# Optimization experiments

Measured on AMD Instinct MI355X. Metric: run time of the kernel, lower is better.

Reference implementation:

```python
import jax, jax.numpy as jnp
import numpy as np

D_MODEL = 1024
NUM_HEADS = 16
D_K = D_MODEL // NUM_HEADS
ROPE_THETA = 10000.0


def setup_inputs() -> dict:
    key = jax.random.key(0)
    kx, kq, kk, kv, ko = jax.random.split(key, 5)
    B, S = 4, 2048
    std = (2.0 / (D_MODEL + D_MODEL)) ** 0.5
    def w(k):
        return jax.random.truncated_normal(k, -3.0, 3.0, (D_MODEL, D_MODEL), jnp.float32) * std
    return {
        "x": jax.random.normal(kx, (B, S, D_MODEL), jnp.float32),
        "Wq": w(kq), "Wk": w(kk), "Wv": w(kv), "Wo": w(ko),
    }


def _apply_rope(t):
    # t: [B, H, S, d_k]
    S, dk = t.shape[-2], t.shape[-1]
    inv_freq = 1.0 / (ROPE_THETA ** (jnp.arange(0, dk, 2) / dk))  # [dk/2]
    angles = jnp.outer(jnp.arange(S), inv_freq)                    # [S, dk/2]
    cos = jnp.repeat(jnp.cos(angles), 2, axis=-1).astype(t.dtype)  # [S, dk]
    sin = jnp.repeat(jnp.sin(angles), 2, axis=-1).astype(t.dtype)
    t_even = t[..., 0::2]
    t_odd = t[..., 1::2]
    t_rot = jnp.stack([-t_odd, t_even], axis=-1).reshape(t.shape)
    return t * cos + t_rot * sin


def reference(x, Wq, Wk, Wv, Wo):
    B, S, D = x.shape
    H, dk = NUM_HEADS, D_K
    q = jnp.einsum("bsi,io->bso", x, Wq).reshape(B, S, H, dk).swapaxes(1, 2)
    k = jnp.einsum("bsi,io->bso", x, Wk).reshape(B, S, H, dk).swapaxes(1, 2)
    v = jnp.einsum("bsi,io->bso", x, Wv).reshape(B, S, H, dk).swapaxes(1, 2)
    q = _apply_rope(q)
    k = _apply_rope(k)
    scores = jnp.einsum("bhqd,bhkd->bhqk", q, k) / (dk ** 0.5)  # [B,H,S,S]
    causal = jnp.tril(jnp.ones((S, S), dtype=bool))
    scores = jnp.where(causal, scores, -jnp.inf)
    attn = jax.nn.softmax(scores, axis=-1)
    out = jnp.einsum("bhqk,bhkd->bhqd", attn, v)  # [B,H,S,dk]
    out = out.swapaxes(1, 2).reshape(B, S, D)
    return jnp.einsum("bsi,io->bso", out, Wo)
```

## Files before the change

### kernel.cpp

```cpp
#include <hip/hip_runtime.h>
#include <hip/hip_bf16.h>

#define SEQ   2048
#define NB    4
#define NH    16
#define DK    64
#define DM    1024
#define MROWS (NB * SEQ)

typedef __bf16 bf16_t;
typedef __bf16 bf16x8 __attribute__((ext_vector_type(8)));
typedef __bf16 bf16x4 __attribute__((ext_vector_type(4)));
typedef float  f32x4  __attribute__((ext_vector_type(4)));

#define MFMA16(a, b, c) __builtin_amdgcn_mfma_f32_16x16x32_bf16((a), (b), (c), 0, 0, 0)

__device__ __forceinline__ void gl2lds16(const bf16_t* g, bf16_t* l) {
    __builtin_amdgcn_global_load_lds(
        (const __attribute__((address_space(1))) unsigned int*)g,
        (__attribute__((address_space(3))) unsigned int*)l, 16, 0, 0);
}

#define BAR()   __builtin_amdgcn_s_barrier()
#define SCB()   __builtin_amdgcn_sched_barrier(0)
#define LGK0()  asm volatile("s_waitcnt lgkmcnt(0)")
#define LGK8()  asm volatile("s_waitcnt lgkmcnt(8)")
#define VMC(N)  asm volatile("s_waitcnt vmcnt(" #N ")")

__global__ __launch_bounds__(256) void cvt_kernel(
    const float* __restrict__ in, bf16_t* __restrict__ out, int n)
{
    int i = (blockIdx.x * 256 + threadIdx.x) * 4;
    if (i + 3 < n) {
        const float4 v = *(const float4*)(in + i);
        bf16x4 o;
        o[0] = (bf16_t)v.x; o[1] = (bf16_t)v.y;
        o[2] = (bf16_t)v.z; o[3] = (bf16_t)v.w;
        *(bf16x4*)(out + i) = o;
    }
}

__global__ __launch_bounds__(256) void wtr_kernel(
    const float* __restrict__ W, bf16_t* __restrict__ Wt)
{
    __shared__ float T[32][33];
    const int tk0 = (blockIdx.x >> 5) << 5;
    const int tn0 = (blockIdx.x & 31) << 5;
    const int r = threadIdx.x >> 5, c = threadIdx.x & 31;
#pragma unroll
    for (int i = 0; i < 4; ++i)
        T[r + i * 8][c] = W[(size_t)(tk0 + r + i * 8) * DM + tn0 + c];
    __syncthreads();
#pragma unroll
    for (int i = 0; i < 4; ++i)
        Wt[(size_t)(tn0 + r + i * 8) * DM + tk0 + c] = (bf16_t)T[c][r + i * 8];
}

__global__ void rope_table_kernel(float2* __restrict__ tab) {
    int idx = blockIdx.x * 256 + threadIdx.x;
    if (idx >= SEQ * 32) return;
    int s = idx >> 5, i = idx & 31;
    float freq = powf(10000.0f, -(float)i / 32.0f);
    float a = (float)s * freq;
    tab[idx] = make_float2(cosf(a), sinf(a));
}

template<bool TR>
__device__ __forceinline__ void kloop(
    const bf16_t* __restrict__ Xp, const bf16_t* __restrict__ Wp,
    bf16_t* L, int tid, f32x4 (&acc)[8][4])
{
    const int lane = tid & 63;
    const int wave = tid >> 6;
    const int wm   = wave >> 2;
    const int wn   = wave & 3;
    const int lrow = lane & 15;
    const int lcol = (lane >> 4) << 3;

    bf16_t* const AR = L;
    bf16_t* const BR = L + 32768;

    const bf16_t* pA0 = Xp + (size_t)(wave * 16 + lrow) * DM + lcol;
    const bf16_t* pA1 = pA0 + (size_t)128 * DM;
    const bf16_t* pB0 = Wp + (size_t)(wave * 16 + lrow) * DM + lcol;
    const bf16_t* pB1 = pB0 + (size_t)128 * DM;

    bf16_t* const adst = AR + wave * 1024;
    bf16_t* const bdst = BR + wave * 1024;

    const bf16_t* const Ard = AR + wm * 8192;
    const bf16_t* const Brd = BR + wn * 4096;

    bf16x8 a[2][2], bc[4][2];

#define RD_A(BUF, Q)                                                          \
    a[0][0] = *(const bf16x8*)(Ard + (BUF) + (2*(Q)+0)*1024 + lane*8);        \
    a[0][1] = *(const bf16x8*)(Ard + (BUF) + (2*(Q)+0)*1024 + 512 + lane*8);  \
    a[1][0] = *(const bf16x8*)(Ard + (BUF) + (2*(Q)+1)*1024 + lane*8);        \
    a[1][1] = *(const bf16x8*)(Ard + (BUF) + (2*(Q)+1)*1024 + 512 + lane*8);

#define RD_B(BUF, NF)                                                         \
    bc[NF][0] = *(const bf16x8*)(Brd + (BUF) + (NF)*1024 + lane*8);           \
    bc[NF][1] = *(const bf16x8*)(Brd + (BUF) + (NF)*1024 + 512 + lane*8);

#define ST_A(BUF, H, C)                                                       \
    gl2lds16(((H) ? pA1 : pA0) + (C),      adst + (BUF) + (H)*8192);          \
    gl2lds16(((H) ? pA1 : pA0) + (C) + 32, adst + (BUF) + (H)*8192 + 512);

#define ST_B(BUF, H, C)                                                       \
    gl2lds16(((H) ? pB1 : pB0) + (C),      bdst + (BUF) + (H)*8192);          \
    gl2lds16(((H) ? pB1 : pB0) + (C) + 32, bdst + (BUF) + (H)*8192 + 512);

#define QMMA(Q)                                                               \
    __builtin_amdgcn_s_setprio(1);                                            \
    _Pragma("unroll")                                                         \
    for (int nf = 0; nf < 4; ++nf) {                                          \
        if (TR) {                                                             \
            acc[2*(Q)][nf]   = MFMA16(bc[nf][0], a[0][0], acc[2*(Q)][nf]);    \
            acc[2*(Q)][nf]   = MFMA16(bc[nf][1], a[0][1], acc[2*(Q)][nf]);    \
            acc[2*(Q)+1][nf] = MFMA16(bc[nf][0], a[1][0], acc[2*(Q)+1][nf]);  \
            acc[2*(Q)+1][nf] = MFMA16(bc[nf][1], a[1][1], acc[2*(Q)+1][nf]);  \
        } else {                                                              \
            acc[2*(Q)][nf]   = MFMA16(a[0][0], bc[nf][0], acc[2*(Q)][nf]);    \
            acc[2*(Q)][nf]   = MFMA16(a[0][1], bc[nf][1], acc[2*(Q)][nf]);    \
            acc[2*(Q)+1][nf] = MFMA16(a[1][0], bc[nf][0], acc[2*(Q)+1][nf]);  \
            acc[2*(Q)+1][nf] = MFMA16(a[1][1], bc[nf][1], acc[2*(Q)+1][nf]);  \
        }                                                                     \
    }                                                                         \
    __builtin_amdgcn_s_setprio(0);

    ST_B(0, 0, 0)      ST_B(0, 1, 0)
    ST_A(0, 0, 0)      ST_A(0, 1, 0)
    ST_B(16384, 0, 64) ST_B(16384, 1, 64)
    VMC(4);
    BAR();

    for (int it = 0; it < 8; ++it) {
        const bool lst = (it == 7);

        RD_A(0, 0) RD_B(0, 0) RD_B(0, 1) RD_B(0, 2) RD_B(0, 3)
        ST_A(16384, 0, 64) ST_A(16384, 1, 64)
        LGK8();
        BAR(); LGK0(); SCB();
        QMMA(0)
        BAR();

        RD_A(0, 1)
        if (!lst) { ST_B(0, 0, 128) }
        BAR(); LGK0(); SCB();
        QMMA(1)
        BAR();

        RD_A(0, 2)
        if (!lst) { ST_B(0, 1, 128) }
        BAR(); LGK0(); SCB();
        QMMA(2)
        BAR();

        RD_A(0, 3)
        BAR(); LGK0(); SCB();
        QMMA(3)
        if (lst) { VMC(0); } else { VMC(4); }
        BAR();

        RD_A(16384, 0) RD_B(16384, 0) RD_B(16384, 1) RD_B(16384, 2) RD_B(16384, 3)
        if (!lst) { ST_A(0, 0, 128) }
        LGK8();
        BAR(); LGK0(); SCB();
        QMMA(0)
        BAR();

        RD_A(16384, 1)
        if (!lst) { ST_A(0, 1, 128) }
        BAR(); LGK0(); SCB();
        QMMA(1)
        BAR();

        RD_A(16384, 2)
        if (!lst) { ST_B(16384, 0, 192) }
        BAR(); LGK0(); SCB();
        QMMA(2)
        BAR();

        RD_A(16384, 3)
        if (!lst) { ST_B(16384, 1, 192) }
        BAR(); LGK0(); SCB();
        QMMA(3)
        if (!lst) { VMC(4); }
        BAR();

        pA0 += 128; pA1 += 128; pB0 += 128; pB1 += 128;
    }

#undef QMMA
#undef ST_B
#undef ST_A
#undef RD_B
#undef RD_A
}

__global__ __launch_bounds__(512, 2) void gemm_qkv_kernel(
    const bf16_t* __restrict__ X, const bf16_t* __restrict__ Wt,
    bf16_t* __restrict__ Qt, bf16_t* __restrict__ Kt, bf16_t* __restrict__ Vtr,
    const float2* __restrict__ rope)
{
    __shared__ __align__(16) bf16_t L[65536];

    const int tid = threadIdx.x;
    const int xcd = blockIdx.x & 7;
    const int idx = blockIdx.x >> 3;
    const int mt  = xcd * 4 + (idx & 3);
    const int nt  = idx >> 2;
    const int m0 = mt << 8, n0 = nt << 8;
    const bool tr = (n0 >= 2 * DM);

    f32x4 acc[8][4] = {};
    if (tr) kloop<true >(X + (size_t)m0 * DM, Wt + (size_t)n0 * DM, L, tid, acc);
    else    kloop<false>(X + (size_t)m0 * DM, Wt + (size_t)n0 * DM, L, tid, acc);

    const int lane = tid & 63;
    const int wave = tid >> 6;
    const int wm   = wave >> 2, wn = wave & 3;
    const int l    = lane & 15;
    const int quad = lane >> 4;

#pragma unroll
    for (int mf = 0; mf < 8; ++mf)
#pragma unroll
        for (int nf = 0; nf < 4; ++nf)
#pragma unroll
            for (int r = 0; r < 4; ++r) {
                float v = acc[mf][nf][r];
                if (tr) {
                    const int n = n0 + wn * 64 + nf * 16 + quad * 4 + r;
                    const int m = m0 + wm * 128 + mf * 16 + l;
                    const int bi = m >> 11, s = m & (SEQ - 1);
                    const int col = n & (DM - 1);
                    const int h = col >> 6, d = col & (DK - 1);
                    Vtr[(((size_t)(bi * NH + h)) * DK + d) * SEQ + s] = (bf16_t)v;
                } else {
                    const int m  = m0 + wm * 128 + mf * 16 + quad * 4 + r;
                    const int nn = n0 + wn * 64 + nf * 16 + l;
                    const int bi = m >> 11, s = m & (SEQ - 1);
                    const int col = nn & (DM - 1);
                    const int h = col >> 6, d = col & (DK - 1);
                    float pv = __shfl_xor(v, 1);
                    float2 cs = rope[s * 32 + (d >> 1)];
                    float res = (d & 1) ? (v * cs.x + pv * cs.y)
                                        : (v * cs.x - pv * cs.y);
                    bf16_t* dst = (nn < DM) ? Qt : Kt;
                    if (nn < DM) res *= 0.125f;
                    dst[(((size_t)(bi * NH + h)) * SEQ + s) * DK + d] = (bf16_t)res;
                }
            }
}

__global__ __launch_bounds__(512, 2) void gemm_out_kernel(
    const bf16_t* __restrict__ X, const bf16_t* __restrict__ Wt,
    float* __restrict__ out)
{
    __shared__ __align__(16) bf16_t L[65536];

    const int tid = threadIdx.x;
    const int xcd = blockIdx.x & 7;
    const int idx = blockIdx.x >> 3;
    const int mt  = xcd * 4 + (idx & 3);
    const int nt  = idx >> 2;
    const int m0 = mt << 8, n0 = nt << 8;

    f32x4 acc[8][4] = {};
    kloop<false>(X + (size_t)m0 * DM, Wt + (size_t)n0 * DM, L, tid, acc);

    const int lane = tid & 63;
    const int wave = tid >> 6;
    const int wm   = wave >> 2, wn = wave & 3;
    const int l    = lane & 15;
    const int quad = lane >> 4;

#pragma unroll
    for (int mf = 0; mf < 8; ++mf)
#pragma unroll
        for (int nf = 0; nf < 4; ++nf)
#pragma unroll
            for (int r = 0; r < 4; ++r) {
                const int m  = m0 + wm * 128 + mf * 16 + quad * 4 + r;
                const int nn = n0 + wn * 64 + nf * 16 + l;
                out[(size_t)m * DM + nn] = acc[mf][nf][r];
            }
}

#define KLD 72

__global__ __launch_bounds__(256) void attn_kernel(
    const bf16_t* __restrict__ Q, const bf16_t* __restrict__ K,
    const bf16_t* __restrict__ Vt, bf16_t* __restrict__ O)
{
    __shared__ __align__(16) bf16_t Kl[64 * KLD];
    __shared__ __align__(16) bf16_t Vl[64 * KLD];
    __shared__ __align__(16) bf16_t Pl[4][32 * KLD];

    const int bh   = blockIdx.x;
    const int qx   = blockIdx.y;
    const int tid  = threadIdx.x;
    const int wave = tid >> 6;
    const int lane = tid & 63;
    const int l    = lane & 15;
    const int quad = lane >> 4;
    const int srow = tid >> 3;
    const int sch  = (tid & 7) << 3;

    bf16_t* Pw = Pl[wave];
    const bf16_t* Qb = Q  + (size_t)bh * SEQ * DK;
    const bf16_t* Kb = K  + (size_t)bh * SEQ * DK;
    const bf16_t* Vb = Vt + (size_t)bh * DK * SEQ;
    const int b = bh >> 4, h = bh & 15;

    for (int ph = 0; ph < 2; ++ph) {
        const int qblk = ph ? (15 - qx) : qx;
        const int q0w  = qblk * 128 + wave * 32;
        const int nch  = 2 * (qblk + 1);

        bf16x8 qb[2][2];
#pragma unroll
        for (int u = 0; u < 2; ++u) {
            qb[u][0] = *(const bf16x8*)(Qb + (size_t)(q0w + u * 16 + l) * DK + quad * 8);
            qb[u][1] = *(const bf16x8*)(Qb + (size_t)(q0w + u * 16 + l) * DK + 32 + quad * 8);
        }

        float m_run[2] = {-3e38f, -3e38f};
        float l_run[2] = {0.f, 0.f};
        f32x4 o[4][2] = {};

        bf16x8 pk0 = *(const bf16x8*)(Kb + (size_t)srow * DK + sch);
        bf16x8 pk1 = *(const bf16x8*)(Kb + (size_t)(32 + srow) * DK + sch);
        bf16x8 pv0 = *(const bf16x8*)(Vb + (size_t)srow * SEQ + sch);
        bf16x8 pv1 = *(const bf16x8*)(Vb + (size_t)(32 + srow) * SEQ + sch);

        for (int i = 0; i < nch; ++i) {
            const int c = i * 64;
            __syncthreads();
            *(bf16x8*)(Kl + srow * KLD + sch)        = pk0;
            *(bf16x8*)(Kl + (32 + srow) * KLD + sch) = pk1;
            *(bf16x8*)(Vl + srow * KLD + sch)        = pv0;
            *(bf16x8*)(Vl + (32 + srow) * KLD + sch) = pv1;
            __syncthreads();
            if (i + 1 < nch) {
                const int cn = c + 64;
                pk0 = *(const bf16x8*)(Kb + (size_t)(cn + srow) * DK + sch);
                pk1 = *(const bf16x8*)(Kb + (size_t)(cn + 32 + srow) * DK + sch);
                pv0 = *(const bf16x8*)(Vb + (size_t)srow * SEQ + cn + sch);
                pv1 = *(const bf16x8*)(Vb + (size_t)(32 + srow) * SEQ + cn + sch);
            }
            if (c > q0w + 31) continue;

            f32x4 st[4][2] = {};
#pragma unroll
            for (int t = 0; t < 4; ++t) {
                const bf16x8 k0 = *(const bf16x8*)(Kl + (t * 16 + l) * KLD + quad * 8);
                const bf16x8 k1 = *(const bf16x8*)(Kl + (t * 16 + l) * KLD + 32 + quad * 8);
                st[t][0] = MFMA16(k0, qb[0][0], st[t][0]);
                st[t][0] = MFMA16(k1, qb[0][1], st[t][0]);
                st[t][1] = MFMA16(k0, qb[1][0], st[t][1]);
                st[t][1] = MFMA16(k1, qb[1][1], st[t][1]);
            }
            if (c + 63 > q0w) {
#pragma unroll
                for (int u = 0; u < 2; ++u) {
                    const int thr = q0w + u * 16 + l - c - quad * 4;
#pragma unroll
                    for (int t = 0; t < 4; ++t)
#pragma unroll
                        for (int r = 0; r < 4; ++r)
                            if (t * 16 + r > thr) st[t][u][r] = -3e38f;
                }
            }
#pragma unroll
            for (int u = 0; u < 2; ++u) {
                float cmax = -3e38f;
#pragma unroll
                for (int t = 0; t < 4; ++t)
#pragma unroll
                    for (int r = 0; r < 4; ++r)
                        cmax = fmaxf(cmax, st[t][u][r]);
                cmax = fmaxf(cmax, __shfl_xor(cmax, 16));
                cmax = fmaxf(cmax, __shfl_xor(cmax, 32));
                const float mnew  = fmaxf(m_run[u], cmax);
                const float alpha = __expf(m_run[u] - mnew);
                m_run[u] = mnew;
                float csum = 0.f;
#pragma unroll
                for (int t = 0; t < 4; ++t)
#pragma unroll
                    for (int r = 0; r < 4; ++r) {
                        st[t][u][r] = __expf(st[t][u][r] - mnew);
                        csum += st[t][u][r];
                    }
                csum += __shfl_xor(csum, 16);
                csum += __shfl_xor(csum, 32);
                l_run[u] = l_run[u] * alpha + csum;
#pragma unroll
                for (int n = 0; n < 4; ++n)
#pragma unroll
                    for (int r = 0; r < 4; ++r)
                        o[n][u][r] *= alpha;
#pragma unroll
                for (int t = 0; t < 4; ++t) {
                    bf16x4 pk;
                    pk[0] = (bf16_t)st[t][u][0]; pk[1] = (bf16_t)st[t][u][1];
                    pk[2] = (bf16_t)st[t][u][2]; pk[3] = (bf16_t)st[t][u][3];
                    *(bf16x4*)(Pw + (u * 16 + l) * KLD + t * 16 + quad * 4) = pk;
                }
            }
            const bf16x8 pb00 = *(const bf16x8*)(Pw + l * KLD + quad * 8);
            const bf16x8 pb01 = *(const bf16x8*)(Pw + l * KLD + 32 + quad * 8);
            const bf16x8 pb10 = *(const bf16x8*)(Pw + (16 + l) * KLD + quad * 8);
            const bf16x8 pb11 = *(const bf16x8*)(Pw + (16 + l) * KLD + 32 + quad * 8);
#pragma unroll
            for (int n = 0; n < 4; ++n) {
                const bf16x8 v0 = *(const bf16x8*)(Vl + (n * 16 + l) * KLD + quad * 8);
                const bf16x8 v1 = *(const bf16x8*)(Vl + (n * 16 + l) * KLD + 32 + quad * 8);
                o[n][0] = MFMA16(v0, pb00, o[n][0]);
                o[n][0] = MFMA16(v1, pb01, o[n][0]);
                o[n][1] = MFMA16(v0, pb10, o[n][1]);
                o[n][1] = MFMA16(v1, pb11, o[n][1]);
            }
        }

#pragma unroll
        for (int u = 0; u < 2; ++u) {
            const float inv = 1.0f / l_run[u];
#pragma unroll
            for (int n = 0; n < 4; ++n) {
                bf16x4 ov;
                ov[0] = (bf16_t)(o[n][u][0] * inv); ov[1] = (bf16_t)(o[n][u][1] * inv);
                ov[2] = (bf16_t)(o[n][u][2] * inv); ov[3] = (bf16_t)(o[n][u][3] * inv);
                *(bf16x4*)(Pw + (u * 16 + l) * KLD + n * 16 + quad * 4) = ov;
            }
        }
        const int row  = lane >> 1;
        const int half = (lane & 1) * 32;
        const bf16x8 w0 = *(const bf16x8*)(Pw + row * KLD + half);
        const bf16x8 w1 = *(const bf16x8*)(Pw + row * KLD + half + 8);
        const bf16x8 w2 = *(const bf16x8*)(Pw + row * KLD + half + 16);
        const bf16x8 w3 = *(const bf16x8*)(Pw + row * KLD + half + 24);
        bf16_t* op = O + ((size_t)(b * SEQ + qblk * 128 + wave * 32 + row)) * DM
                       + h * DK + half;
        *(bf16x8*)(op)      = w0;
        *(bf16x8*)(op + 8)  = w1;
        *(bf16x8*)(op + 16) = w2;
        *(bf16x8*)(op + 24) = w3;
    }
}

extern "C" void kernel_launch(void* const* d_in, const int* in_sizes, int n_in,
                              void* d_out, int out_size, void* d_ws, size_t ws_size,
                              hipStream_t stream)
{
    const float* x  = (const float*)d_in[0];
    const float* Wq = (const float*)d_in[1];
    const float* Wk = (const float*)d_in[2];
    const float* Wv = (const float*)d_in[3];
    const float* Wo = (const float*)d_in[4];

    char* ws = (char*)d_ws;
    float2* rope = (float2*)ws;
    const size_t TEN = (size_t)MROWS * DM;
    const size_t WEL = (size_t)DM * DM;
    bf16_t* xb    = (bf16_t*)(ws + (1 << 19));
    bf16_t* Wqkvt = xb + TEN;
    bf16_t* Wot   = Wqkvt + 3 * WEL;
    bf16_t* Qt    = Wot + WEL;
    bf16_t* Kt    = Qt + TEN;
    bf16_t* Vt    = Kt + TEN;
    bf16_t* Ot    = Vt + TEN;

    rope_table_kernel<<<(SEQ * 32 + 255) / 256, 256, 0, stream>>>(rope);

    cvt_kernel<<<(int)(TEN / 4 / 256), 256, 0, stream>>>(x, xb, (int)TEN);
    wtr_kernel<<<1024, 256, 0, stream>>>(Wq, Wqkvt);
    wtr_kernel<<<1024, 256, 0, stream>>>(Wk, Wqkvt + WEL);
    wtr_kernel<<<1024, 256, 0, stream>>>(Wv, Wqkvt + 2 * WEL);
    wtr_kernel<<<1024, 256, 0, stream>>>(Wo, Wot);

    gemm_qkv_kernel<<<32 * 12, 512, 0, stream>>>(xb, Wqkvt, Qt, Kt, Vt, rope);

    attn_kernel<<<dim3(NB * NH, 8), 256, 0, stream>>>(Qt, Kt, Vt, Ot);

    gemm_out_kernel<<<32 * 4, 512, 0, stream>>>(Ot, Wot, (float*)d_out);
}
```

Baseline: 310.3 us.

## Merge prep kernels, halve output GEMM tile, double-buffer attention K/V

Replaces the six setup launches (rope table, x conversion, four weight transposes) with a single prep kernel that dispatches on block index. The output projection GEMM moves from 256x256 to 128x256 tiles with its own inlined pipelined k-loop, doubling the block count from 128 to 256 so more CUs are busy. The attention kernel double-buffers K/V in shared memory so it needs one barrier per chunk instead of two. The costs are more LDS in attention, less reuse per block in the output GEMM, and a more complex hand-written barrier/waitcnt schedule.

```diff
diff --git a/kernel.cpp b/kernel.cpp
--- a/kernel.cpp
+++ b/kernel.cpp
@@ -7,6 +7,7 @@
 #define DK    64
 #define DM    1024
 #define MROWS (NB * SEQ)
+#define WEL   (DM * DM)
 
 typedef __bf16 bf16_t;
 typedef __bf16 bf16x8 __attribute__((ext_vector_type(8)));
@@ -27,42 +28,47 @@
 #define LGK8()  asm volatile("s_waitcnt lgkmcnt(8)")
 #define VMC(N)  asm volatile("s_waitcnt vmcnt(" #N ")")
 
-__global__ __launch_bounds__(256) void cvt_kernel(
-    const float* __restrict__ in, bf16_t* __restrict__ out, int n)
+__global__ __launch_bounds__(256) void prep_kernel(
+    const float* __restrict__ x,
+    const float* __restrict__ Wq, const float* __restrict__ Wk,
+    const float* __restrict__ Wv, const float* __restrict__ Wo,
+    bf16_t* __restrict__ xb, bf16_t* __restrict__ Wqkvt,
+    bf16_t* __restrict__ Wot, float2* __restrict__ rope)
 {
-    int i = (blockIdx.x * 256 + threadIdx.x) * 4;
-    if (i + 3 < n) {
-        const float4 v = *(const float4*)(in + i);
+    __shared__ float T[32][33];
+    const int bid = blockIdx.x;
+    const int tid = threadIdx.x;
+
+    if (bid < 8192) {
+        const int i = (bid * 256 + tid) * 4;
+        const float4 v = *(const float4*)(x + i);
         bf16x4 o;
         o[0] = (bf16_t)v.x; o[1] = (bf16_t)v.y;
         o[2] = (bf16_t)v.z; o[3] = (bf16_t)v.w;
-        *(bf16x4*)(out + i) = o;
+        *(bf16x4*)(xb + i) = o;
+    } else if (bid < 12288) {
+        const int wb = bid - 8192;
+        const int w  = wb >> 10;
+        const int b10 = wb & 1023;
+        const float* W = (w == 0) ? Wq : (w == 1) ? Wk : (w == 2) ? Wv : Wo;
+        bf16_t* Wt = (w == 3) ? Wot : Wqkvt + (size_t)w * WEL;
+        const int tk0 = (b10 >> 5) << 5;
+        const int tn0 = (b10 & 31) << 5;
+        const int r = tid >> 5, c = tid & 31;
+#pragma unroll
+        for (int i = 0; i < 4; ++i)
+            T[r + i * 8][c] = W[(size_t)(tk0 + r + i * 8) * DM + tn0 + c];
+        __syncthreads();
+#pragma unroll
+        for (int i = 0; i < 4; ++i)
+            Wt[(size_t)(tn0 + r + i * 8) * DM + tk0 + c] = (bf16_t)T[c][r + i * 8];
+    } else {
+        const int idx = (bid - 12288) * 256 + tid;
+        const int s = idx >> 5, i = idx & 31;
+        const float freq = powf(10000.0f, -(float)i / 32.0f);
+        const float a = (float)s * freq;
+        rope[idx] = make_float2(cosf(a), sinf(a));
     }
-}
-
-__global__ __launch_bounds__(256) void wtr_kernel(
-    const float* __restrict__ W, bf16_t* __restrict__ Wt)
-{
-    __shared__ float T[32][33];
-    const int tk0 = (blockIdx.x >> 5) << 5;
-    const int tn0 = (blockIdx.x & 31) << 5;
-    const int r = threadIdx.x >> 5, c = threadIdx.x & 31;
-#pragma unroll
-    for (int i = 0; i < 4; ++i)
-        T[r + i * 8][c] = W[(size_t)(tk0 + r + i * 8) * DM + tn0 + c];
-    __syncthreads();
-#pragma unroll
-    for (int i = 0; i < 4; ++i)
-        Wt[(size_t)(tn0 + r + i * 8) * DM + tk0 + c] = (bf16_t)T[c][r + i * 8];
-}
-
-__global__ void rope_table_kernel(float2* __restrict__ tab) {
-    int idx = blockIdx.x * 256 + threadIdx.x;
-    if (idx >= SEQ * 32) return;
-    int s = idx >> 5, i = idx & 31;
-    float freq = powf(10000.0f, -(float)i / 32.0f);
-    float a = (float)s * freq;
-    tab[idx] = make_float2(cosf(a), sinf(a));
 }
 
 template<bool TR>
@@ -259,44 +265,136 @@
     const bf16_t* __restrict__ X, const bf16_t* __restrict__ Wt,
     float* __restrict__ out)
 {
-    __shared__ __align__(16) bf16_t L[65536];
+    __shared__ __align__(16) bf16_t L[49152];
 
     const int tid = threadIdx.x;
     const int xcd = blockIdx.x & 7;
     const int idx = blockIdx.x >> 3;
-    const int mt  = xcd * 4 + (idx & 3);
-    const int nt  = idx >> 2;
-    const int m0 = mt << 8, n0 = nt << 8;
-
-    f32x4 acc[8][4] = {};
-    kloop<false>(X + (size_t)m0 * DM, Wt + (size_t)n0 * DM, L, tid, acc);
+    const int mt  = xcd * 8 + (idx & 7);
+    const int nt  = idx >> 3;
+    const int m0 = mt << 7, n0 = nt << 8;
 
     const int lane = tid & 63;
     const int wave = tid >> 6;
-    const int wm   = wave >> 2, wn = wave & 3;
+    const int wm   = wave >> 2;
+    const int wn   = wave & 3;
+    const int lrow = lane & 15;
+    const int lcol = (lane >> 4) << 3;
+
+    bf16_t* const AR = L;
+    bf16_t* const BR = L + 16384;
+
+    const bf16_t* Xp = X + (size_t)m0 * DM;
+    const bf16_t* Wp = Wt + (size_t)n0 * DM;
+    const bf16_t* pA  = Xp + (size_t)(wave * 16 + lrow) * DM + lcol;
+    const bf16_t* pB0 = Wp + (size_t)(wave * 16 + lrow) * DM + lcol;
+    const bf16_t* pB1 = pB0 + (size_t)128 * DM;
+
+    bf16_t* const adst = AR + wave * 1024;
+    bf16_t* const bdst = BR + wave * 1024;
+
+    const bf16_t* const Ard = AR + wm * 4096;
+    const bf16_t* const Brd = BR + wn * 4096;
+
+    f32x4 acc[4][4] = {};
+    bf16x8 a[2][2], bc[4][2];
+
+#define RD_AH(BUF, Q)                                                         \
+    a[0][0] = *(const bf16x8*)(Ard + (BUF) + (2*(Q)+0)*1024 + lane*8);        \
+    a[0][1] = *(const bf16x8*)(Ard + (BUF) + (2*(Q)+0)*1024 + 512 + lane*8);  \
+    a[1][0] = *(const bf16x8*)(Ard + (BUF) + (2*(Q)+1)*1024 + lane*8);        \
+    a[1][1] = *(const bf16x8*)(Ard + (BUF) + (2*(Q)+1)*1024 + 512 + lane*8);
+
+#define RD_BH(BUF, NF)                                                        \
+    bc[NF][0] = *(const bf16x8*)(Brd + (BUF) + (NF)*1024 + lane*8);           \
+    bc[NF][1] = *(const bf16x8*)(Brd + (BUF) + (NF)*1024 + 512 + lane*8);
+
+#define ST_AH(BUF, C)                                                         \
+    gl2lds16(pA + (C),      adst + (BUF));                                    \
+    gl2lds16(pA + (C) + 32, adst + (BUF) + 512);
+
+#define ST_BH(BUF, H, C)                                                      \
+    gl2lds16(((H) ? pB1 : pB0) + (C),      bdst + (BUF) + (H)*8192);          \
+    gl2lds16(((H) ? pB1 : pB0) + (C) + 32, bdst + (BUF) + (H)*8192 + 512);
+
+#define QMMAH(Q)                                                              \
+    __builtin_amdgcn_s_setprio(1);                                            \
+    _Pragma("unroll")                                                         \
+    for (int nf = 0; nf < 4; ++nf) {                                          \
+        acc[2*(Q)][nf]   = MFMA16(a[0][0], bc[nf][0], acc[2*(Q)][nf]);        \
+        acc[2*(Q)][nf]   = MFMA16(a[0][1], bc[nf][1], acc[2*(Q)][nf]);        \
+        acc[2*(Q)+1][nf] = MFMA16(a[1][0], bc[nf][0], acc[2*(Q)+1][nf]);      \
+        acc[2*(Q)+1][nf] = MFMA16(a[1][1], bc[nf][1], acc[2*(Q)+1][nf]);      \
+    }                                                                         \
+    __builtin_amdgcn_s_setprio(0);
+
+    ST_AH(0, 0)
+    ST_BH(0, 0, 0) ST_BH(0, 1, 0)
+    ST_BH(16384, 0, 64) ST_BH(16384, 1, 64)
+    VMC(4);
+    BAR();
+
+    for (int it = 0; it < 8; ++it) {
+        const bool lst = (it == 7);
+
+        RD_AH(0, 0) RD_BH(0, 0) RD_BH(0, 1) RD_BH(0, 2) RD_BH(0, 3)
+        ST_AH(8192, 64)
+        LGK8();
+        BAR(); LGK0(); SCB();
+        QMMAH(0)
+        BAR();
+        RD_AH(0, 1)
+        if (!lst) { ST_BH(0, 0, 128) ST_BH(0, 1, 128) }
+        BAR(); LGK0(); SCB();
+        QMMAH(1)
+        if (lst) { VMC(0); } else { VMC(4); }
+        BAR();
+
+        RD_AH(8192, 0) RD_BH(16384, 0) RD_BH(16384, 1) RD_BH(16384, 2) RD_BH(16384, 3)
+        if (!lst) { ST_AH(0, 128) }
+        LGK8();
+        BAR(); LGK0(); SCB();
+        QMMAH(0)
+        BAR();
+        RD_AH(8192, 1)
+        if (!lst) { ST_BH(16384, 0, 192) ST_BH(16384, 1, 192) }
+        BAR(); LGK0(); SCB();
+        QMMAH(1)
+        if (!lst) { VMC(4); }
+        BAR();
+
+        pA += 128; pB0 += 128; pB1 += 128;
+    }
+
+#undef QMMAH
+#undef ST_BH
+#undef ST_AH
+#undef RD_BH
+#undef RD_AH
+
     const int l    = lane & 15;
     const int quad = lane >> 4;
-
-#pragma unroll
-    for (int mf = 0; mf < 8; ++mf)
+#pragma unroll
+    for (int mf = 0; mf < 4; ++mf)
 #pragma unroll
         for (int nf = 0; nf < 4; ++nf)
 #pragma unroll
             for (int r = 0; r < 4; ++r) {
-                const int m  = m0 + wm * 128 + mf * 16 + quad * 4 + r;
+                const int m  = m0 + wm * 64 + mf * 16 + quad * 4 + r;
                 const int nn = n0 + wn * 64 + nf * 16 + l;
                 out[(size_t)m * DM + nn] = acc[mf][nf][r];
             }
 }
 
-#define KLD 72
+#define KLD  72
+#define KVSZ (64 * KLD)
 
 __global__ __launch_bounds__(256) void attn_kernel(
     const bf16_t* __restrict__ Q, const bf16_t* __restrict__ K,
     const bf16_t* __restrict__ Vt, bf16_t* __restrict__ O)
 {
-    __shared__ __align__(16) bf16_t Kl[64 * KLD];
-    __shared__ __align__(16) bf16_t Vl[64 * KLD];
+    __shared__ __align__(16) bf16_t Kl[2 * KVSZ];
+    __shared__ __align__(16) bf16_t Vl[2 * KVSZ];
     __shared__ __align__(16) bf16_t Pl[4][32 * KLD];
 
     const int bh   = blockIdx.x;
@@ -335,95 +433,111 @@
         bf16x8 pk1 = *(const bf16x8*)(Kb + (size_t)(32 + srow) * DK + sch);
         bf16x8 pv0 = *(const bf16x8*)(Vb + (size_t)srow * SEQ + sch);
         bf16x8 pv1 = *(const bf16x8*)(Vb + (size_t)(32 + srow) * SEQ + sch);
+        __syncthreads();
+        *(bf16x8*)(Kl + srow * KLD + sch)        = pk0;
+        *(bf16x8*)(Kl + (32 + srow) * KLD + sch) = pk1;
+        *(bf16x8*)(Vl + srow * KLD + sch)        = pv0;
+        *(bf16x8*)(Vl + (32 + srow) * KLD + sch) = pv1;
+        __syncthreads();
 
         for (int i = 0; i < nch; ++i) {
-            const int c = i * 64;
-            __syncthreads();
-            *(bf16x8*)(Kl + srow * KLD + sch)        = pk0;
-            *(bf16x8*)(Kl + (32 + srow) * KLD + sch) = pk1;
-            *(bf16x8*)(Vl + srow * KLD + sch)        = pv0;
-            *(bf16x8*)(Vl + (32 + srow) * KLD + sch) = pv1;
-            __syncthreads();
-            if (i + 1 < nch) {
+            const int c  = i * 64;
+            const int bf = (i & 1) * KVSZ;
+            const int bn = ((i & 1) ^ 1) * KVSZ;
+            const bool pf = (i + 1 < nch);
+
+            if (pf) {
                 const int cn = c + 64;
                 pk0 = *(const bf16x8*)(Kb + (size_t)(cn + srow) * DK + sch);
                 pk1 = *(const bf16x8*)(Kb + (size_t)(cn + 32 + srow) * DK + sch);
                 pv0 = *(const bf16x8*)(Vb + (size_t)srow * SEQ + cn + sch);
                 pv1 = *(const bf16x8*)(Vb + (size_t)(32 + srow) * SEQ + cn + sch);
             }
-            if (c > q0w + 31) continue;
-
-            f32x4 st[4][2] = {};
-#pragma unroll
-            for (int t = 0; t < 4; ++t) {
-                const bf16x8 k0 = *(const bf16x8*)(Kl + (t * 16 + l) * KLD + quad * 8);
-                const bf16x8 k1 = *(const bf16x8*)(Kl + (t * 16 + l) * KLD + 32 + quad * 8);
-                st[t][0] = MFMA16(k0, qb[0][0], st[t][0]);
-                st[t][0] = MFMA16(k1, qb[0][1], st[t][0]);
-                st[t][1] = MFMA16(k0, qb[1][0], st[t][1]);
-                st[t][1] = MFMA16(k1, qb[1][1], st[t][1]);
-            }
-            if (c + 63 > q0w) {
+
+            if (c <= q0w + 31) {
+                const bf16_t* Klb = Kl + bf;
+                const bf16_t* Vlb = Vl + bf;
+
+                f32x4 st[4][2] = {};
+#pragma unroll
+                for (int t = 0; t < 4; ++t) {
+                    const bf16x8 k0 = *(const bf16x8*)(Klb + (t * 16 + l) * KLD + quad * 8);
+                    const bf16x8 k1 = *(const bf16x8*)(Klb + (t * 16 + l) * KLD + 32 + quad * 8);
+                    st[t][0] = MFMA16(k0, qb[0][0], st[t][0]);
+                    st[t][0] = MFMA16(k1, qb[0][1], st[t][0]);
+                    st[t][1] = MFMA16(k0, qb[1][0], st[t][1]);
+                    st[t][1] = MFMA16(k1, qb[1][1], st[t][1]);
+                }
+                if (c + 63 > q0w) {
+#pragma unroll
+                    for (int u = 0; u < 2; ++u) {
+                        const int thr = q0w + u * 16 + l - c - quad * 4;
+#pragma unroll
+                        for (int t = 0; t < 4; ++t)
+#pragma unroll
+                            for (int r = 0; r < 4; ++r)
+                                if (t * 16 + r > thr) st[t][u][r] = -3e38f;
+                    }
+                }
 #pragma unroll
                 for (int u = 0; u < 2; ++u) {
-                    const int thr = q0w + u * 16 + l - c - quad * 4;
+                    float cmax = -3e38f;
 #pragma unroll
                     for (int t = 0; t < 4; ++t)
 #pragma unroll
                         for (int r = 0; r < 4; ++r)
-                            if (t * 16 + r > thr) st[t][u][r] = -3e38f;
+                            cmax = fmaxf(cmax, st[t][u][r]);
+                    cmax = fmaxf(cmax, __shfl_xor(cmax, 16));
+                    cmax = fmaxf(cmax, __shfl_xor(cmax, 32));
+                    const float mnew  = fmaxf(m_run[u], cmax);
+                    const float alpha = __expf(m_run[u] - mnew);
+                    m_run[u] = mnew;
+                    float csum = 0.f;
+#pragma unroll
+                    for (int t = 0; t < 4; ++t)
+#pragma unroll
+                        for (int r = 0; r < 4; ++r) {
+                            st[t][u][r] = __expf(st[t][u][r] - mnew);
+                            csum += st[t][u][r];
+                        }
+                    csum += __shfl_xor(csum, 16);
+                    csum += __shfl_xor(csum, 32);
+                    l_run[u] = l_run[u] * alpha + csum;
+#pragma unroll
+                    for (int n = 0; n < 4; ++n)
+#pragma unroll
+                        for (int r = 0; r < 4; ++r)
+                            o[n][u][r] *= alpha;
+#pragma unroll
+                    for (int t = 0; t < 4; ++t) {
+                        bf16x4 pk;
+                        pk[0] = (bf16_t)st[t][u][0]; pk[1] = (bf16_t)st[t][u][1];
+                        pk[2] = (bf16_t)st[t][u][2]; pk[3] = (bf16_t)st[t][u][3];
+                        *(bf16x4*)(Pw + (u * 16 + l) * KLD + t * 16 + quad * 4) = pk;
+                    }
+                }
+                const bf16x8 pb00 = *(const bf16x8*)(Pw + l * KLD + quad * 8);
+                const bf16x8 pb01 = *(const bf16x8*)(Pw + l * KLD + 32 + quad * 8);
+                const bf16x8 pb10 = *(const bf16x8*)(Pw + (16 + l) * KLD + quad * 8);
+                const bf16x8 pb11 = *(const bf16x8*)(Pw + (16 + l) * KLD + 32 + quad * 8);
+#pragma unroll
+                for (int n = 0; n < 4; ++n) {
+                    const bf16x8 v0 = *(const bf16x8*)(Vlb + (n * 16 + l) * KLD + quad * 8);
+                    const bf16x8 v1 = *(const bf16x8*)(Vlb + (n * 16 + l) * KLD + 32 + quad * 8);
+                    o[n][0] = MFMA16(v0, pb00, o[n][0]);
+                    o[n][0] = MFMA16(v1, pb01, o[n][0]);
+                    o[n][1] = MFMA16(v0, pb10, o[n][1]);
+                    o[n][1] = MFMA16(v1, pb11, o[n][1]);
                 }
             }
-#pragma unroll
-            for (int u = 0; u < 2; ++u) {
-                float cmax = -3e38f;
-#pragma unroll
-                for (int t = 0; t < 4; ++t)
-#pragma unroll
-                    for (int r = 0; r < 4; ++r)
-                        cmax = fmaxf(cmax, st[t][u][r]);
-                cmax = fmaxf(cmax, __shfl_xor(cmax, 16));
-                cmax = fmaxf(cmax, __shfl_xor(cmax, 32));
-                const float mnew  = fmaxf(m_run[u], cmax);
-                const float alpha = __expf(m_run[u] - mnew);
-                m_run[u] = mnew;
-                float csum = 0.f;
-#pragma unroll
-                for (int t = 0; t < 4; ++t)
-#pragma unroll
-                    for (int r = 0; r < 4; ++r) {
-                        st[t][u][r] = __expf(st[t][u][r] - mnew);
-                        csum += st[t][u][r];
-                    }
-                csum += __shfl_xor(csum, 16);
-                csum += __shfl_xor(csum, 32);
-                l_run[u] = l_run[u] * alpha + csum;
-#pragma unroll
-                for (int n = 0; n < 4; ++n)
-#pragma unroll
-                    for (int r = 0; r < 4; ++r)
-                        o[n][u][r] *= alpha;
-#pragma unroll
-                for (int t = 0; t < 4; ++t) {
-                    bf16x4 pk;
-                    pk[0] = (bf16_t)st[t][u][0]; pk[1] = (bf16_t)st[t][u][1];
-                    pk[2] = (bf16_t)st[t][u][2]; pk[3] = (bf16_t)st[t][u][3];
-                    *(bf16x4*)(Pw + (u * 16 + l) * KLD + t * 16 + quad * 4) = pk;
-                }
+
+            if (pf) {
+                *(bf16x8*)(Kl + bn + srow * KLD + sch)        = pk0;
+                *(bf16x8*)(Kl + bn + (32 + srow) * KLD + sch) = pk1;
+                *(bf16x8*)(Vl + bn + srow * KLD + sch)        = pv0;
+                *(bf16x8*)(Vl + bn + (32 + srow) * KLD + sch) = pv1;
             }
-            const bf16x8 pb00 = *(const bf16x8*)(Pw + l * KLD + quad * 8);
-            const bf16x8 pb01 = *(const bf16x8*)(Pw + l * KLD + 32 + quad * 8);
-            const bf16x8 pb10 = *(const bf16x8*)(Pw + (16 + l) * KLD + quad * 8);
-            const bf16x8 pb11 = *(const bf16x8*)(Pw + (16 + l) * KLD + 32 + quad * 8);
-#pragma unroll
-            for (int n = 0; n < 4; ++n) {
-                const bf16x8 v0 = *(const bf16x8*)(Vl + (n * 16 + l) * KLD + quad * 8);
-                const bf16x8 v1 = *(const bf16x8*)(Vl + (n * 16 + l) * KLD + 32 + quad * 8);
-                o[n][0] = MFMA16(v0, pb00, o[n][0]);
-                o[n][0] = MFMA16(v1, pb01, o[n][0]);
-                o[n][1] = MFMA16(v0, pb10, o[n][1]);
-                o[n][1] = MFMA16(v1, pb11, o[n][1]);
-            }
+            __syncthreads();
         }
 
 #pragma unroll
@@ -465,26 +579,20 @@
     char* ws = (char*)d_ws;
     float2* rope = (float2*)ws;
     const size_t TEN = (size_t)MROWS * DM;
-    const size_t WEL = (size_t)DM * DM;
     bf16_t* xb    = (bf16_t*)(ws + (1 << 19));
     bf16_t* Wqkvt = xb + TEN;
-    bf16_t* Wot   = Wqkvt + 3 * WEL;
+    bf16_t* Wot   = Wqkvt + 3 * (size_t)WEL;
     bf16_t* Qt    = Wot + WEL;
     bf16_t* Kt    = Qt + TEN;
     bf16_t* Vt    = Kt + TEN;
     bf16_t* Ot    = Vt + TEN;
 
-    rope_table_kernel<<<(SEQ * 32 + 255) / 256, 256, 0, stream>>>(rope);
-
-    cvt_kernel<<<(int)(TEN / 4 / 256), 256, 0, stream>>>(x, xb, (int)TEN);
-    wtr_kernel<<<1024, 256, 0, stream>>>(Wq, Wqkvt);
-    wtr_kernel<<<1024, 256, 0, stream>>>(Wk, Wqkvt + WEL);
-    wtr_kernel<<<1024, 256, 0, stream>>>(Wv, Wqkvt + 2 * WEL);
-    wtr_kernel<<<1024, 256, 0, stream>>>(Wo, Wot);
+    prep_kernel<<<12544, 256, 0, stream>>>(x, Wq, Wk, Wv, Wo,
+                                           xb, Wqkvt, Wot, rope);
 
     gemm_qkv_kernel<<<32 * 12, 512, 0, stream>>>(xb, Wqkvt, Qt, Kt, Vt, rope);
 
     attn_kernel<<<dim3(NB * NH, 8), 256, 0, stream>>>(Qt, Kt, Vt, Ot);
 
-    gemm_out_kernel<<<32 * 4, 512, 0, stream>>>(Ot, Wot, (float*)d_out);
-}
+    gemm_out_kernel<<<64 * 4, 512, 0, stream>>>(Ot, Wot, (float*)d_out);
+}
```

After: 299.3 us. 1.04x faster.
